# Kernel tuning notes

Measured on AMD Instinct MI355X. Metric: run time of the kernel, lower is better.

Reference implementation:

```python
import jax, jax.numpy as jnp
import numpy as np

H = 512  # hidden_size


def setup_inputs() -> dict:
    key = jax.random.key(0)
    ks = jax.random.split(key, 8)
    B, L = 16, 2048
    query = jax.random.normal(ks[0], (B, 1, 2 * H), dtype=jnp.float32)
    keys = jax.random.normal(ks[1], (B, L, 2 * H), dtype=jnp.float32)
    coverage = jax.random.uniform(ks[2], (B, L, 1), dtype=jnp.float32)
    # alignment MLP: Linear(4H+1 -> 2H, bias) -> tanh -> Linear(2H -> 1, no bias) -> softmax(dim=1)
    s1 = 1.0 / np.sqrt(4 * H + 1)
    W1 = jax.random.uniform(ks[3], (4 * H + 1, 2 * H), jnp.float32, -s1, s1)
    b1 = jax.random.uniform(ks[4], (2 * H,), jnp.float32, -s1, s1)
    s2 = 1.0 / np.sqrt(2 * H)
    W2 = jax.random.uniform(ks[5], (2 * H, 1), jnp.float32, -s2, s2)
    # reduce: Linear(2H -> H, no bias)
    Wr = jax.random.uniform(ks[6], (2 * H, H), jnp.float32, -s2, s2)
    return {"query": query, "keys": keys, "coverage": coverage,
            "W1": W1, "b1": b1, "W2": W2, "Wr": Wr}


def reference(query, keys, coverage, W1, b1, W2, Wr):
    B, L, _ = keys.shape
    q = jnp.broadcast_to(query, (B, L, query.shape[-1]))          # (B,L,2H)
    feat = jnp.concatenate([q, keys, coverage], axis=-1)          # (B,L,4H+1)
    h = jnp.tanh(feat @ W1 + b1)                                  # (B,L,2H)
    scores = h @ W2                                               # (B,L,1)
    attention = jax.nn.softmax(scores, axis=1)                    # softmax over length
    reduced = keys @ Wr                                           # (B,L,H)
    context = jnp.einsum('blo,blh->boh', attention, reduced)      # (B,1,H)
    return context, attention
```

## Files before the change

kernel.cpp:

```cpp
#include <hip/hip_runtime.h>
#include <hip/hip_bf16.h>
#include <stdint.h>

typedef short bf16x8 __attribute__((ext_vector_type(8)));
typedef float f32x4 __attribute__((ext_vector_type(4)));
typedef unsigned int u32x2 __attribute__((ext_vector_type(2)));
typedef unsigned int u32x4 __attribute__((ext_vector_type(4)));

__device__ __forceinline__ uint32_t pack2f(float lo, float hi) {
  union { __hip_bfloat162 h; uint32_t u; } c;
  c.h.x = __float2bfloat16(lo);
  c.h.y = __float2bfloat16(hi);
  return c.u;
}

__device__ __forceinline__ unsigned short f32_to_bf16(float f) {
  union { __hip_bfloat16 h; unsigned short u; } c;
  c.h = __float2bfloat16(f);
  return c.u;
}

__device__ __forceinline__ float bfbits_to_f32(uint32_t hi16) {
  union { uint32_t u; float f; } c;
  c.u = hi16 << 16;
  return c.f;
}

__device__ __forceinline__ float fast_tanh(float x) {
  float e = __builtin_amdgcn_exp2f(x * 2.8853900817779268f);
  return 1.0f - 2.0f * __builtin_amdgcn_rcpf(e + 1.0f);
}

#define GLD16(g, l)                                                                    \
  __builtin_amdgcn_global_load_lds((const __attribute__((address_space(1))) void*)(g), \
                                   (__attribute__((address_space(3))) void*)(l), 16, 0, 0)

#define MFMA16(a, b, c) __builtin_amdgcn_mfma_f32_16x16x32_bf16(a, b, c, 0, 0, 0)
#define SBAR0() __builtin_amdgcn_sched_barrier(0)

__global__ void prep_kernel(const float* __restrict__ keys, unsigned short* __restrict__ keysbf,
                            const float* __restrict__ W1, unsigned short* __restrict__ W1kt,
                            const float* __restrict__ query, const float* __restrict__ b1,
                            float* __restrict__ qterm) {
  __shared__ __align__(16) unsigned char smem[16896];
  const int bid = blockIdx.x;
  const int t = threadIdx.x;
  if (bid < 256) {
    float (*tt)[65] = (float(*)[65])smem;
    const int kb = (bid & 15) * 64;
    const int jb = (bid >> 4) * 64;
    const int c = t & 63;
    const int r = t >> 6;
#pragma unroll
    for (int i = 0; i < 16; ++i) {
      const int k = i * 4 + r;
      tt[k][c] = W1[(size_t)(1024 + kb + k) * 1024 + (jb + c)];
    }
    __syncthreads();
#pragma unroll
    for (int i = 0; i < 16; ++i) {
      const int j = i * 4 + r;
      W1kt[(size_t)(jb + j) * 1024 + (kb + c)] = f32_to_bf16(tt[c][j]);
    }
  } else if (bid < 512) {
    float (*part)[64] = (float(*)[64])smem;
    const int q = bid - 256;
    const int b = q >> 4;
    const int j = (q & 15) * 64 + (t & 63);
    const int kq = t >> 6;
    const float* qp = query + b * 1024 + kq * 256;
    const float* wp = W1 + (size_t)(kq * 256) * 1024 + j;
    float acc = 0.f;
#pragma unroll 8
    for (int k = 0; k < 256; ++k) acc += qp[k] * wp[(size_t)k * 1024];
    part[kq][t & 63] = acc;
    __syncthreads();
    if (t < 64) {
      const int jj = (q & 15) * 64 + t;
      qterm[b * 1024 + jj] = b1[jj] + part[0][t] + part[1][t] + part[2][t] + part[3][t];
    }
  } else {
    const size_t base = (size_t)(bid - 512) * 16384;
#pragma unroll
    for (int bt = 0; bt < 2; ++bt) {
      f32x4 v[8];
#pragma unroll
      for (int i = 0; i < 8; ++i)
        v[i] = *(const f32x4*)(keys + base + bt * 8192 + i * 1024 + t * 4);
#pragma unroll
      for (int i = 0; i < 8; ++i) {
        u32x2 p;
        p.x = pack2f(v[i].x, v[i].y);
        p.y = pack2f(v[i].z, v[i].w);
        *(u32x2*)(keysbf + base + bt * 8192 + i * 1024 + t * 4) = p;
      }
    }
  }
}


#define V12_STAGE(kt_, P)                                                           \
  _Pragma("unroll") for (int i = 0; i < 2; ++i) {                                   \
    const int r = i * 128 + w * 16 + (lane >> 2);                                   \
    const int u = (lane & 3) ^ ((r >> 1) & 3);                                      \
    GLD16(keysbf + (size_t)(row0 + r) * 1024 + (kt_) * 32 + u * 8,                  \
          (P) + i * 8192 + w * 1024 + lane * 16);                                   \
    GLD16(W1kt + (size_t)(col0 + r) * 1024 + (kt_) * 32 + u * 8,                    \
          (P) + 16384 + i * 8192 + w * 1024 + lane * 16);                           \
  }

#define V12_COMPUTE(P)                                                              \
  {                                                                                 \
    bf16x8 af[8], bfv[4];                                                           \
    _Pragma("unroll") for (int mf = 0; mf < 8; ++mf) {                              \
      const int ra = wm * 128 + mf * 16 + c16;                                      \
      af[mf] = *(const bf16x8*)((P) + ra * 64 + ((q4 ^ ((ra >> 1) & 3)) << 4));     \
    }                                                                               \
    _Pragma("unroll") for (int nf = 0; nf < 4; ++nf) {                              \
      const int ca = wn * 64 + nf * 16 + c16;                                       \
      bfv[nf] =                                                                     \
          *(const bf16x8*)((P) + 16384 + ca * 64 + ((q4 ^ ((ca >> 1) & 3)) << 4));  \
    }                                                                               \
    __builtin_amdgcn_s_setprio(1);                                                  \
    _Pragma("unroll") for (int nf = 0; nf < 4; ++nf)                                \
        _Pragma("unroll") for (int mf = 0; mf < 8; ++mf) acc[mf][nf] =              \
            MFMA16(af[mf], bfv[nf], acc[mf][nf]);                                   \
    __builtin_amdgcn_s_setprio(0);                                                  \
  }

#define V12_ITER(ts_, Pc, Ps)                             \
  asm volatile("s_waitcnt vmcnt(4)" ::: "memory");        \
  __builtin_amdgcn_s_barrier();                           \
  SBAR0();                                                \
  V12_STAGE(ts_, Ps);                                     \
  V12_COMPUTE(Pc);

__global__ __launch_bounds__(512, 2) void gemm_score_v12(
    const unsigned short* __restrict__ keysbf, const unsigned short* __restrict__ W1kt,
    const float* __restrict__ qterm, const float* __restrict__ coverage,
    const float* __restrict__ W1, const float* __restrict__ W2,
    float* __restrict__ scores_part) {
  __shared__ __align__(16) unsigned char lds[102400];
  unsigned char* P0 = lds;
  unsigned char* P1 = lds + 32768;
  unsigned char* P2 = lds + 65536;
  float* Sred = (float*)(lds + 98304);

  const int tid = threadIdx.x;
  const int bid = blockIdx.x;
  const int xcd = bid & 7;
  const int idx = bid >> 3;
  const int rowt = xcd * 16 + (idx >> 2);
  const int colgrp = idx & 3;
  const int row0 = rowt * 256;
  const int col0 = colgrp * 256;
  const int b = row0 >> 11;
  const int w = tid >> 6;
  const int wm = w >> 2, wn = w & 3;
  const int lane = tid & 63;
  const int c16 = lane & 15, q4 = lane >> 4;

  f32x4 acc[8][4];
  const f32x4 zz = {0.f, 0.f, 0.f, 0.f};
#pragma unroll
  for (int mf = 0; mf < 8; ++mf)
#pragma unroll
    for (int nf = 0; nf < 4; ++nf) acc[mf][nf] = zz;

  V12_STAGE(0, P0);
  V12_STAGE(1, P1);

#pragma unroll 1
  for (int tb = 0; tb < 30; tb += 3) {
    V12_ITER(tb + 2, P0, P2);
    V12_ITER(tb + 3, P1, P0);
    V12_ITER(tb + 4, P2, P1);
  }
  asm volatile("s_waitcnt vmcnt(4)" ::: "memory");
  __builtin_amdgcn_s_barrier();
  SBAR0();
  V12_COMPUTE(P0);
  asm volatile("s_waitcnt vmcnt(0)" ::: "memory");
  __builtin_amdgcn_s_barrier();
  SBAR0();
  V12_COMPUTE(P1);

  float covv[8][4];
#pragma unroll
  for (int mf = 0; mf < 8; ++mf)
#pragma unroll
    for (int r = 0; r < 4; ++r)
      covv[mf][r] = coverage[row0 + wm * 128 + mf * 16 + q4 * 4 + r];

  float p_part[8][4];
#pragma unroll
  for (int mf = 0; mf < 8; ++mf)
#pragma unroll
    for (int r = 0; r < 4; ++r) p_part[mf][r] = 0.f;

#pragma unroll
  for (int nf = 0; nf < 4; ++nf) {
    const int col = col0 + wn * 64 + nf * 16 + c16;
    const float qt = qterm[b * 1024 + col];
    const float w1c = W1[(size_t)2048 * 1024 + col];
    const float w2 = W2[col];
#pragma unroll
    for (int mf = 0; mf < 8; ++mf)
#pragma unroll
      for (int r = 0; r < 4; ++r) {
        float v = acc[mf][nf][r] + qt + covv[mf][r] * w1c;
        p_part[mf][r] += fast_tanh(v) * w2;
      }
  }

#pragma unroll
  for (int mf = 0; mf < 8; ++mf)
#pragma unroll
    for (int r = 0; r < 4; ++r) {
      float p = p_part[mf][r];
      p += __shfl_xor(p, 1);
      p += __shfl_xor(p, 2);
      p += __shfl_xor(p, 4);
      p += __shfl_xor(p, 8);
      if (c16 == 0) Sred[w * 128 + mf * 16 + q4 * 4 + r] = p;
    }
  __syncthreads();
  if (tid < 256) {
    const int wmv = tid >> 7, rl = tid & 127;
    float s = Sred[(wmv * 4 + 0) * 128 + rl] + Sred[(wmv * 4 + 1) * 128 + rl] +
              Sred[(wmv * 4 + 2) * 128 + rl] + Sred[(wmv * 4 + 3) * 128 + rl];
    scores_part[(size_t)colgrp * 32768 + row0 + tid] = s;
  }
}

__global__ void softmax_kernel(const float* __restrict__ sp, float* __restrict__ att) {
  const int b = blockIdx.x;
  const int tid = threadIdx.x;
  float* a = att + b * 2048;
  __shared__ float red[4];
  float mx = -1e30f;
  for (int l = tid; l < 2048; l += 256) {
    float v = 0.f;
#pragma unroll
    for (int g = 0; g < 4; ++g) v += sp[(size_t)g * 32768 + b * 2048 + l];
    a[l] = v;
    mx = fmaxf(mx, v);
  }
#pragma unroll
  for (int o = 1; o < 64; o <<= 1) mx = fmaxf(mx, __shfl_xor(mx, o));
  if ((tid & 63) == 0) red[tid >> 6] = mx;
  __syncthreads();
  mx = fmaxf(fmaxf(red[0], red[1]), fmaxf(red[2], red[3]));
  __syncthreads();
  float sum = 0.f;
  for (int l = tid; l < 2048; l += 256) {
    float e = __expf(a[l] - mx);
    a[l] = e;
    sum += e;
  }
#pragma unroll
  for (int o = 1; o < 64; o <<= 1) sum += __shfl_xor(sum, o);
  if ((tid & 63) == 0) red[tid >> 6] = sum;
  __syncthreads();
  sum = red[0] + red[1] + red[2] + red[3];
  const float inv = 1.0f / sum;
  for (int l = tid; l < 2048; l += 256) a[l] *= inv;
}

__global__ void ctxpre_kernel(const unsigned short* __restrict__ keysbf,
                              const float* __restrict__ att, float* __restrict__ ctx_part) {
  const int b = blockIdx.x;
  const int sl = blockIdx.y;
  const int tid = threadIdx.x;
  const float* ab = att + b * 2048 + sl * 128;
  const unsigned short* kb = keysbf + ((size_t)b * 2048 + sl * 128) * 1024 + tid * 4;
  f32x4 acc = {0.f, 0.f, 0.f, 0.f};
#pragma unroll 4
  for (int l = 0; l < 128; ++l) {
    u32x2 v = *(const u32x2*)(kb + (size_t)l * 1024);
    const float al = ab[l];
    acc.x += bfbits_to_f32(v.x & 0xFFFFu) * al;
    acc.y += bfbits_to_f32(v.x >> 16) * al;
    acc.z += bfbits_to_f32(v.y & 0xFFFFu) * al;
    acc.w += bfbits_to_f32(v.y >> 16) * al;
  }
  *(f32x4*)(ctx_part + ((size_t)(sl * 16 + b)) * 1024 + tid * 4) = acc;
}

__global__ void ctx2_kernel(const float* __restrict__ ctx_part, const float* __restrict__ Wr,
                            float* __restrict__ out) {
  __shared__ float cpre[1024];
  __shared__ float part[4][64];
  const int hb = blockIdx.x;
  const int b = blockIdx.y;
  const int t = threadIdx.x;
#pragma unroll
  for (int jj = 0; jj < 4; ++jj) {
    const int j = jj * 256 + t;
    float s = 0.f;
#pragma unroll
    for (int sl = 0; sl < 16; ++sl) s += ctx_part[((size_t)(sl * 16 + b)) * 1024 + j];
    cpre[j] = s;
  }
  __syncthreads();
  const int h = hb * 64 + (t & 63);
  const int jq = t >> 6;
  const float* wp = Wr + (size_t)(jq * 256) * 512 + h;
  float acc = 0.f;
#pragma unroll 8
  for (int k = 0; k < 256; ++k) acc += cpre[jq * 256 + k] * wp[(size_t)k * 512];
  part[jq][t & 63] = acc;
  __syncthreads();
  if (t < 64)
    out[b * 512 + hb * 64 + t] = part[0][t] + part[1][t] + part[2][t] + part[3][t];
}

extern "C" void kernel_launch(void* const* d_in, const int* in_sizes, int n_in, void* d_out,
                              int out_size, void* d_ws, size_t ws_size, hipStream_t stream) {
  const float* query = (const float*)d_in[0];
  const float* keys = (const float*)d_in[1];
  const float* coverage = (const float*)d_in[2];
  const float* W1 = (const float*)d_in[3];
  const float* b1 = (const float*)d_in[4];
  const float* W2 = (const float*)d_in[5];
  const float* Wr = (const float*)d_in[6];
  float* out = (float*)d_out;
  char* ws = (char*)d_ws;

  float* scores_part = (float*)ws;
  float* ctx_part = (float*)ws;
  float* qterm = (float*)(ws + 1114112);
  unsigned short* W1kt = (unsigned short*)(ws + 1179648);
  unsigned short* keysbf = (unsigned short*)(ws + 3276800);

  float* context_out = out;
  float* att_out = out + 8192;

  prep_kernel<<<dim3(2560), dim3(256), 0, stream>>>(keys, keysbf, W1, W1kt, query, b1, qterm);
  gemm_score_v12<<<dim3(512), dim3(512), 0, stream>>>(keysbf, W1kt, qterm, coverage, W1, W2,
                                                      scores_part);
  softmax_kernel<<<dim3(16), dim3(256), 0, stream>>>(scores_part, att_out);
  ctxpre_kernel<<<dim3(16, 16), dim3(256), 0, stream>>>(keysbf, att_out, ctx_part);
  ctx2_kernel<<<dim3(8, 16), dim3(256), 0, stream>>>(ctx_part, Wr, context_out);
}
```

Measured before the change: 141.6 us.

## Use K=64 double-buffered GEMM stages and fuse softmax into context kernel

The score GEMM moves from a triple-buffered K=32 pipeline with partial vmcnt waits to a double-buffered K=64 pipeline. It also uses a new XOR swizzle and precomputed global and LDS addresses, so there are half as many barrier iterations. In exchange, each iteration now waits fully (vmcnt(0)) and uses more LDS per block. Separately, the softmax kernel is fused into the context pre-reduction kernel: each of the 256 blocks recomputes the full softmax max and sum for its batch and keeps its slice of attention in shared memory. This removes one launch and a global round trip, at the cost of redundant reductions. The workspace layout is also changed so ctx_part no longer aliases scores_part.

```diff
diff --git a/kernel.cpp b/kernel.cpp
--- a/kernel.cpp
+++ b/kernel.cpp
@@ -5,7 +5,6 @@
 typedef short bf16x8 __attribute__((ext_vector_type(8)));
 typedef float f32x4 __attribute__((ext_vector_type(4)));
 typedef unsigned int u32x2 __attribute__((ext_vector_type(2)));
-typedef unsigned int u32x4 __attribute__((ext_vector_type(4)));
 
 __device__ __forceinline__ uint32_t pack2f(float lo, float hi) {
   union { __hip_bfloat162 h; uint32_t u; } c;
@@ -99,52 +98,51 @@
 }
 
 
-#define V12_STAGE(kt_, P)                                                           \
-  _Pragma("unroll") for (int i = 0; i < 2; ++i) {                                   \
-    const int r = i * 128 + w * 16 + (lane >> 2);                                   \
-    const int u = (lane & 3) ^ ((r >> 1) & 3);                                      \
-    GLD16(keysbf + (size_t)(row0 + r) * 1024 + (kt_) * 32 + u * 8,                  \
-          (P) + i * 8192 + w * 1024 + lane * 16);                                   \
-    GLD16(W1kt + (size_t)(col0 + r) * 1024 + (kt_) * 32 + u * 8,                    \
-          (P) + 16384 + i * 8192 + w * 1024 + lane * 16);                           \
-  }
-
-#define V12_COMPUTE(P)                                                              \
-  {                                                                                 \
-    bf16x8 af[8], bfv[4];                                                           \
-    _Pragma("unroll") for (int mf = 0; mf < 8; ++mf) {                              \
-      const int ra = wm * 128 + mf * 16 + c16;                                      \
-      af[mf] = *(const bf16x8*)((P) + ra * 64 + ((q4 ^ ((ra >> 1) & 3)) << 4));     \
-    }                                                                               \
-    _Pragma("unroll") for (int nf = 0; nf < 4; ++nf) {                              \
-      const int ca = wn * 64 + nf * 16 + c16;                                       \
-      bfv[nf] =                                                                     \
-          *(const bf16x8*)((P) + 16384 + ca * 64 + ((q4 ^ ((ca >> 1) & 3)) << 4));  \
-    }                                                                               \
-    __builtin_amdgcn_s_setprio(1);                                                  \
-    _Pragma("unroll") for (int nf = 0; nf < 4; ++nf)                                \
-        _Pragma("unroll") for (int mf = 0; mf < 8; ++mf) acc[mf][nf] =              \
-            MFMA16(af[mf], bfv[nf], acc[mf][nf]);                                   \
-    __builtin_amdgcn_s_setprio(0);                                                  \
-  }
-
-#define V12_ITER(ts_, Pc, Ps)                             \
-  asm volatile("s_waitcnt vmcnt(4)" ::: "memory");        \
-  __builtin_amdgcn_s_barrier();                           \
-  SBAR0();                                                \
-  V12_STAGE(ts_, Ps);                                     \
-  V12_COMPUTE(Pc);
-
-__global__ __launch_bounds__(512, 2) void gemm_score_v12(
+#define V16_STAGE(kt_, P)                                            \
+  GLD16(gkA + (kt_) * 64 + 0 * 65536, (P) + 0 * 8192 + t16);         \
+  GLD16(gwB + (kt_) * 64 + 0 * 65536, (P) + 32768 + 0 * 8192 + t16); \
+  GLD16(gkA + (kt_) * 64 + 1 * 65536, (P) + 1 * 8192 + t16);         \
+  GLD16(gwB + (kt_) * 64 + 1 * 65536, (P) + 32768 + 1 * 8192 + t16); \
+  GLD16(gkA + (kt_) * 64 + 2 * 65536, (P) + 2 * 8192 + t16);         \
+  GLD16(gwB + (kt_) * 64 + 2 * 65536, (P) + 32768 + 2 * 8192 + t16); \
+  GLD16(gkA + (kt_) * 64 + 3 * 65536, (P) + 3 * 8192 + t16);         \
+  GLD16(gwB + (kt_) * 64 + 3 * 65536, (P) + 32768 + 3 * 8192 + t16);
+
+#define V16_COMPUTE(P)                                                           \
+  _Pragma("unroll") for (int kk = 0; kk < 2; ++kk) {                             \
+    bf16x8 af[8], bfv[4];                                                        \
+    _Pragma("unroll") for (int mf = 0; mf < 8; ++mf)                             \
+        af[mf] = *(const bf16x8*)((P) + ((abase + mf * 2048) ^ (kk * 64)));      \
+    _Pragma("unroll") for (int nf = 0; nf < 4; ++nf)                             \
+        bfv[nf] = *(const bf16x8*)((P) + ((bbase + nf * 2048) ^ (kk * 64)));     \
+    __builtin_amdgcn_s_setprio(1);                                               \
+    _Pragma("unroll") for (int nf = 0; nf < 4; ++nf)                             \
+        _Pragma("unroll") for (int mf = 0; mf < 8; ++mf) acc[mf][nf] =           \
+            MFMA16(af[mf], bfv[nf], acc[mf][nf]);                                \
+    __builtin_amdgcn_s_setprio(0);                                               \
+  }
+
+#define V16_ITER(t_, Pc, Ps, LAST)                            \
+  asm volatile("s_waitcnt vmcnt(0) lgkmcnt(0)" ::: "memory"); \
+  __builtin_amdgcn_s_barrier();                               \
+  SBAR0();                                                    \
+  if (!(LAST)) { V16_STAGE((t_) + 1, Ps); }                   \
+  SBAR0();                                                    \
+  V16_COMPUTE(Pc);
+
+#define V16_PAIR(t0, t1)      \
+  V16_ITER(t0, P0, P1, false) \
+  V16_ITER(t1, P1, P0, (t1) == 15)
+
+__global__ __launch_bounds__(512, 2) void gemm_score_v16(
     const unsigned short* __restrict__ keysbf, const unsigned short* __restrict__ W1kt,
     const float* __restrict__ qterm, const float* __restrict__ coverage,
     const float* __restrict__ W1, const float* __restrict__ W2,
     float* __restrict__ scores_part) {
-  __shared__ __align__(16) unsigned char lds[102400];
+  __shared__ __align__(16) unsigned char lds[135168];
   unsigned char* P0 = lds;
-  unsigned char* P1 = lds + 32768;
-  unsigned char* P2 = lds + 65536;
-  float* Sred = (float*)(lds + 98304);
+  unsigned char* P1 = lds + 65536;
+  float* Sred = (float*)(lds + 131072);
 
   const int tid = threadIdx.x;
   const int bid = blockIdx.x;
@@ -160,6 +158,16 @@
   const int lane = tid & 63;
   const int c16 = lane & 15, q4 = lane >> 4;
 
+  const int swzc = (q4 ^ (c16 & 7)) << 4;
+  const int abase = (wm * 128 + c16) * 128 + swzc;
+  const int bbase = 32768 + (wn * 64 + c16) * 128 + swzc;
+
+  const int sr = tid >> 3;
+  const int su = (tid & 7) ^ (sr & 7);
+  const unsigned short* gkA = keysbf + (size_t)(row0 + sr) * 1024 + su * 8;
+  const unsigned short* gwB = W1kt + (size_t)(col0 + sr) * 1024 + su * 8;
+  const int t16 = tid * 16;
+
   f32x4 acc[8][4];
   const f32x4 zz = {0.f, 0.f, 0.f, 0.f};
 #pragma unroll
@@ -167,23 +175,16 @@
 #pragma unroll
     for (int nf = 0; nf < 4; ++nf) acc[mf][nf] = zz;
 
-  V12_STAGE(0, P0);
-  V12_STAGE(1, P1);
-
-#pragma unroll 1
-  for (int tb = 0; tb < 30; tb += 3) {
-    V12_ITER(tb + 2, P0, P2);
-    V12_ITER(tb + 3, P1, P0);
-    V12_ITER(tb + 4, P2, P1);
-  }
-  asm volatile("s_waitcnt vmcnt(4)" ::: "memory");
-  __builtin_amdgcn_s_barrier();
-  SBAR0();
-  V12_COMPUTE(P0);
-  asm volatile("s_waitcnt vmcnt(0)" ::: "memory");
-  __builtin_amdgcn_s_barrier();
-  SBAR0();
-  V12_COMPUTE(P1);
+  V16_STAGE(0, P0);
+
+  V16_PAIR(0, 1)
+  V16_PAIR(2, 3)
+  V16_PAIR(4, 5)
+  V16_PAIR(6, 7)
+  V16_PAIR(8, 9)
+  V16_PAIR(10, 11)
+  V16_PAIR(12, 13)
+  V16_PAIR(14, 15)
 
   float covv[8][4];
 #pragma unroll
@@ -233,17 +234,21 @@
   }
 }
 
-__global__ void softmax_kernel(const float* __restrict__ sp, float* __restrict__ att) {
+__global__ void ctxpre_fused(const unsigned short* __restrict__ keysbf,
+                             const float* __restrict__ sp, float* __restrict__ att,
+                             float* __restrict__ ctx_part) {
+  __shared__ float sc[2048];
+  __shared__ float red[4];
+  __shared__ float att_s[128];
   const int b = blockIdx.x;
+  const int sl = blockIdx.y;
   const int tid = threadIdx.x;
-  float* a = att + b * 2048;
-  __shared__ float red[4];
   float mx = -1e30f;
   for (int l = tid; l < 2048; l += 256) {
     float v = 0.f;
 #pragma unroll
     for (int g = 0; g < 4; ++g) v += sp[(size_t)g * 32768 + b * 2048 + l];
-    a[l] = v;
+    sc[l] = v;
     mx = fmaxf(mx, v);
   }
 #pragma unroll
@@ -253,32 +258,25 @@
   mx = fmaxf(fmaxf(red[0], red[1]), fmaxf(red[2], red[3]));
   __syncthreads();
   float sum = 0.f;
-  for (int l = tid; l < 2048; l += 256) {
-    float e = __expf(a[l] - mx);
-    a[l] = e;
-    sum += e;
-  }
+  for (int l = tid; l < 2048; l += 256) sum += __expf(sc[l] - mx);
 #pragma unroll
   for (int o = 1; o < 64; o <<= 1) sum += __shfl_xor(sum, o);
   if ((tid & 63) == 0) red[tid >> 6] = sum;
   __syncthreads();
-  sum = red[0] + red[1] + red[2] + red[3];
-  const float inv = 1.0f / sum;
-  for (int l = tid; l < 2048; l += 256) a[l] *= inv;
-}
-
-__global__ void ctxpre_kernel(const unsigned short* __restrict__ keysbf,
-                              const float* __restrict__ att, float* __restrict__ ctx_part) {
-  const int b = blockIdx.x;
-  const int sl = blockIdx.y;
-  const int tid = threadIdx.x;
-  const float* ab = att + b * 2048 + sl * 128;
+  const float inv = 1.0f / (red[0] + red[1] + red[2] + red[3]);
+  if (tid < 128) {
+    const float a = __expf(sc[sl * 128 + tid] - mx) * inv;
+    att_s[tid] = a;
+    att[b * 2048 + sl * 128 + tid] = a;
+  }
+  __syncthreads();
+
   const unsigned short* kb = keysbf + ((size_t)b * 2048 + sl * 128) * 1024 + tid * 4;
   f32x4 acc = {0.f, 0.f, 0.f, 0.f};
 #pragma unroll 4
   for (int l = 0; l < 128; ++l) {
     u32x2 v = *(const u32x2*)(kb + (size_t)l * 1024);
-    const float al = ab[l];
+    const float al = att_s[l];
     acc.x += bfbits_to_f32(v.x & 0xFFFFu) * al;
     acc.y += bfbits_to_f32(v.x >> 16) * al;
     acc.z += bfbits_to_f32(v.y & 0xFFFFu) * al;
@@ -328,18 +326,17 @@
   char* ws = (char*)d_ws;
 
   float* scores_part = (float*)ws;
-  float* ctx_part = (float*)ws;
-  float* qterm = (float*)(ws + 1114112);
-  unsigned short* W1kt = (unsigned short*)(ws + 1179648);
-  unsigned short* keysbf = (unsigned short*)(ws + 3276800);
+  float* ctx_part = (float*)(ws + 524288);
+  float* qterm = (float*)(ws + 1638400);
+  unsigned short* W1kt = (unsigned short*)(ws + 1703936);
+  unsigned short* keysbf = (unsigned short*)(ws + 3801088);
 
   float* context_out = out;
   float* att_out = out + 8192;
 
   prep_kernel<<<dim3(2560), dim3(256), 0, stream>>>(keys, keysbf, W1, W1kt, query, b1, qterm);
-  gemm_score_v12<<<dim3(512), dim3(512), 0, stream>>>(keysbf, W1kt, qterm, coverage, W1, W2,
+  gemm_score_v16<<<dim3(512), dim3(512), 0, stream>>>(keysbf, W1kt, qterm, coverage, W1, W2,
                                                       scores_part);
-  softmax_kernel<<<dim3(16), dim3(256), 0, stream>>>(scores_part, att_out);
-  ctxpre_kernel<<<dim3(16, 16), dim3(256), 0, stream>>>(keysbf, att_out, ctx_part);
+  ctxpre_fused<<<dim3(16, 16), dim3(256), 0, stream>>>(keysbf, scores_part, att_out, ctx_part);
   ctx2_kernel<<<dim3(8, 16), dim3(256), 0, stream>>>(ctx_part, Wr, context_out);
 }
```

After: 131.4 us. -7.2%, faster.
